# Optimization experiments

Measured on AMD Instinct MI355X. Metric: run time of the kernel, lower is better.

The kernel has to match this reference:

```python
import jax, jax.numpy as jnp
import numpy as np

B, S, D, H, E, K = 4, 1024, 1024, 4096, 8, 2


def setup_inputs() -> dict:
    key = jax.random.key(0)
    ks = jax.random.split(key, 10)
    s = 0.02
    return {
        "x": jax.random.normal(ks[0], (B, S, D), jnp.float32),
        "noise": jax.random.normal(ks[1], (B, S, E), jnp.float32),
        "Wg": jax.random.normal(ks[2], (D, E), jnp.float32) * s,
        "bg": jnp.zeros((E,), jnp.float32),
        "Wn": jax.random.normal(ks[3], (D, E), jnp.float32) * s,
        "bn": jnp.zeros((E,), jnp.float32),
        "W1": jax.random.normal(ks[4], (E, D, H), jnp.float32) * s,
        "b1": jnp.zeros((E, H), jnp.float32),
        "W2": jax.random.normal(ks[5], (E, H, D), jnp.float32) * s,
        "b2": jnp.zeros((E, D), jnp.float32),
    }


def reference(x, noise, Wg, bg, Wn, bn, W1, b1, W2, b2):
    # --- noisy top-k gating ---
    logits = x @ Wg + bg                                   # [B,S,E]
    noisy = logits + noise * jax.nn.softplus(x @ Wn + bn)  # [B,S,E]
    topk_vals, topk_idx = jax.lax.top_k(noisy, K)          # [B,S,K]
    weights = jax.nn.softmax(topk_vals, axis=-1)           # [B,S,K]
    oh = jax.nn.one_hot(topk_idx, E, dtype=x.dtype)        # [B,S,K,E]
    mask = oh.sum(axis=-2)                                 # [B,S,E] 0/1 (topk idx distinct)
    w_full = (weights[..., None] * oh).sum(axis=-2)        # [B,S,E] combine weights

    # --- per-expert FFN (dense over experts, selected via w_full) ---
    h = jax.nn.gelu(jnp.einsum('bsd,edh->bseh', x, W1) + b1, approximate=False)
    eout = jnp.einsum('bseh,ehd->bsed', h, W2) + b2        # [B,S,E,D]
    combined = jnp.einsum('bse,bsed->bsd', w_full, eout)   # [B,S,D]

    # --- load balancing loss on clean gate probs ---
    gate_probs = jax.nn.softmax(logits, axis=-1)           # [B,S,E]
    expert_count = mask.sum(axis=(0, 1))                   # [E]
    total_tokens = mask.sum()
    expert_util = expert_count / total_tokens
    load_loss = jnp.sum(expert_util * gate_probs.mean(axis=(0, 1))) * E
    return combined, load_loss
```

## Files before the change

kernel.cpp:

```cpp
#include <hip/hip_runtime.h>
#include <hip/hip_bf16.h>

#define T_TOK 4096
#define D_DIM 1024
#define H_DIM 4096
#define E_EXP 8
#define K_TOP 2
#define TP (T_TOK * K_TOP)
#define BM 128
#define BN 128
#define BKS 32
#define MAX_TILES 72

typedef __attribute__((ext_vector_type(8))) short bf16x8;
typedef __attribute__((ext_vector_type(4))) float f32x4;
typedef __attribute__((ext_vector_type(8))) unsigned short u16x8;
typedef __attribute__((ext_vector_type(4))) unsigned short u16x4;

#define SWZ(row, chunk) ((chunk) ^ (((row) >> 1) & 3))

static __device__ __forceinline__ void gload16(const unsigned short* g, unsigned short* l) {
  __builtin_amdgcn_global_load_lds((const __attribute__((address_space(1))) void*)g,
                                   (__attribute__((address_space(3))) void*)l, 16, 0, 0);
}

static __device__ __forceinline__ unsigned short f2bf(float f) {
  unsigned int bits = __float_as_uint(f);
  unsigned int lsb = (bits >> 16) & 1u;
  bits += 0x7fffu + lsb;
  return (unsigned short)(bits >> 16);
}

static __device__ __forceinline__ float gelu_fast(float u) {
  float z = u * (0.79788456080286536f + 0.0356774081f * u * u);
  float t = __expf(-2.f * z);
  return u / (1.f + t);
}

__global__ __launch_bounds__(256) void convert_x_kernel(
    const float* __restrict__ x, unsigned short* __restrict__ xb) {
  int idx = blockIdx.x * 256 + threadIdx.x;
  float4 v = ((const float4*)x)[idx];
  u16x4 o;
  o[0] = f2bf(v.x); o[1] = f2bf(v.y); o[2] = f2bf(v.z); o[3] = f2bf(v.w);
  *(u16x4*)(xb + (size_t)idx * 4) = o;
}

__global__ __launch_bounds__(256) void transpose_bf16_kernel(
    const float* __restrict__ src, unsigned short* __restrict__ dst, int R, int C) {
  __shared__ float tile[32][33];
  const int e = blockIdx.z;
  const int c0 = blockIdx.x * 32, r0 = blockIdx.y * 32;
  const int tx = threadIdx.x, ty = threadIdx.y;
  const float* s = src + (size_t)e * R * C;
  unsigned short* d = dst + (size_t)e * R * C;
#pragma unroll
  for (int j = 0; j < 4; ++j)
    tile[ty + 8 * j][tx] = s[(size_t)(r0 + ty + 8 * j) * C + c0 + tx];
  __syncthreads();
#pragma unroll
  for (int j = 0; j < 4; ++j)
    d[(size_t)(c0 + ty + 8 * j) * R + r0 + tx] = f2bf(tile[tx][ty + 8 * j]);
}

__global__ __launch_bounds__(256) void gating_kernel(
    const float* __restrict__ x, const float* __restrict__ noise,
    const float* __restrict__ Wg, const float* __restrict__ bg,
    const float* __restrict__ Wn, const float* __restrict__ bn,
    int* __restrict__ tok_e, float* __restrict__ tok_w,
    float* __restrict__ gp_tok, int* __restrict__ counts) {
  const int tid = threadIdx.x, lane = tid & 63, wid = tid >> 6;
  const int t = blockIdx.x * 4 + wid;
  const float* xrow = x + (size_t)t * D_DIM;
  float ag[8] = {0, 0, 0, 0, 0, 0, 0, 0};
  float an[8] = {0, 0, 0, 0, 0, 0, 0, 0};
#pragma unroll 4
  for (int i = 0; i < 16; ++i) {
    int dd = i * 64 + lane;
    float xv = xrow[dd];
    const float4* g4 = (const float4*)(Wg + (size_t)dd * 8);
    const float4* n4 = (const float4*)(Wn + (size_t)dd * 8);
    float4 ga = g4[0], gb = g4[1], na = n4[0], nb = n4[1];
    ag[0] += xv * ga.x; ag[1] += xv * ga.y; ag[2] += xv * ga.z; ag[3] += xv * ga.w;
    ag[4] += xv * gb.x; ag[5] += xv * gb.y; ag[6] += xv * gb.z; ag[7] += xv * gb.w;
    an[0] += xv * na.x; an[1] += xv * na.y; an[2] += xv * na.z; an[3] += xv * na.w;
    an[4] += xv * nb.x; an[5] += xv * nb.y; an[6] += xv * nb.z; an[7] += xv * nb.w;
  }
#pragma unroll
  for (int e = 0; e < 8; ++e) {
    for (int off = 32; off > 0; off >>= 1) {
      ag[e] += __shfl_down(ag[e], off);
      an[e] += __shfl_down(an[e], off);
    }
  }
  if (lane == 0) {
    float logit[8], noisy[8];
#pragma unroll
    for (int e = 0; e < 8; ++e) {
      logit[e] = ag[e] + bg[e];
      float pre = an[e] + bn[e];
      float sp = fmaxf(pre, 0.f) + log1pf(expf(-fabsf(pre)));
      noisy[e] = logit[e] + noise[(size_t)t * 8 + e] * sp;
    }
    float mx = logit[0];
#pragma unroll
    for (int e = 1; e < 8; ++e) mx = fmaxf(mx, logit[e]);
    float s = 0.f, p[8];
#pragma unroll
    for (int e = 0; e < 8; ++e) { p[e] = expf(logit[e] - mx); s += p[e]; }
    float inv = 1.f / s;
#pragma unroll
    for (int e = 0; e < 8; ++e) gp_tok[(size_t)t * 8 + e] = p[e] * inv;
    int i0 = 0; float v0 = noisy[0];
#pragma unroll
    for (int e = 1; e < 8; ++e) if (noisy[e] > v0) { v0 = noisy[e]; i0 = e; }
    int i1 = -1; float v1 = 0.f;
#pragma unroll
    for (int e = 0; e < 8; ++e) {
      if (e == i0) continue;
      if (i1 < 0 || noisy[e] > v1) { v1 = noisy[e]; i1 = e; }
    }
    float e1 = expf(v1 - v0);
    float w0 = 1.f / (1.f + e1);
    float w1 = e1 * w0;
    tok_e[t * 2 + 0] = i0; tok_e[t * 2 + 1] = i1;
    tok_w[t * 2 + 0] = w0; tok_w[t * 2 + 1] = w1;
    atomicAdd(&counts[i0], 1);
    atomicAdd(&counts[i1], 1);
  }
}

__global__ void scan_kernel(const int* __restrict__ counts, int* __restrict__ offsets,
                            int* __restrict__ cursor, int4* __restrict__ tiles,
                            int* __restrict__ ntiles) {
  if (threadIdx.x == 0 && blockIdx.x == 0) {
    int off = 0, nt = 0;
    for (int e = 0; e < E_EXP; ++e) {
      offsets[e] = off;
      int c = counts[e];
      for (int r = 0; r < c; r += BM) {
        tiles[nt] = make_int4(e, off + r, min(BM, c - r), 0);
        ++nt;
      }
      off += c;
      cursor[e] = 0;
    }
    offsets[E_EXP] = off;
    *ntiles = nt;
  }
}

__global__ __launch_bounds__(256) void scatter_kernel(
    const int* __restrict__ tok_e, const float* __restrict__ tok_w,
    const int* __restrict__ offsets, int* __restrict__ cursor,
    int* __restrict__ pair_token, float* __restrict__ pair_w) {
  int t = blockIdx.x * 256 + threadIdx.x;
  if (t >= T_TOK) return;
#pragma unroll
  for (int k = 0; k < 2; ++k) {
    int e = tok_e[t * 2 + k];
    int pos = atomicAdd(&cursor[e], 1);
    int p = offsets[e] + pos;
    pair_token[p] = t;
    pair_w[p] = tok_w[t * 2 + k];
  }
}

__global__ __launch_bounds__(256) void ffn1_kernel(
    const unsigned short* __restrict__ xb,
    const unsigned short* __restrict__ w1t,
    const float* __restrict__ b1,
    const int* __restrict__ pair_token,
    const int4* __restrict__ tiles, const int* __restrict__ ntiles,
    unsigned short* __restrict__ hbuf) {
  const int NB = H_DIM / BN;
  const int nwg = MAX_TILES * NB;
  int bid = blockIdx.x;
  int wg = (bid & 7) * (nwg >> 3) + (bid >> 3);
  int tileId = wg / NB, nb = wg - tileId * NB;
  if (tileId >= *ntiles) return;
  int4 tl = tiles[tileId];
  const int e = tl.x, row0 = tl.y, rows = tl.z;
  const int n0 = nb * BN;

  __shared__ unsigned short As[BM * BKS];
  __shared__ unsigned short Bs[BN * BKS];

  const int tid = threadIdx.x;
  const int wid = tid >> 6, lane = tid & 63;
  const int sr = tid >> 2;
  const int sc = tid & 3;
  const int scz = SWZ(sr, sc) * 8;

  int r0a = row0 + sr;       if (r0a > TP - 1) r0a = TP - 1;
  int r1a = row0 + sr + 64;  if (r1a > TP - 1) r1a = TP - 1;
  const unsigned short* a0 = xb + (size_t)pair_token[r0a] * D_DIM + scz;
  const unsigned short* a1 = xb + (size_t)pair_token[r1a] * D_DIM + scz;
  const unsigned short* bp0 = w1t + ((size_t)e * H_DIM + (n0 + sr)) * D_DIM + scz;
  const unsigned short* bp1 = w1t + ((size_t)e * H_DIM + (n0 + sr + 64)) * D_DIM + scz;

  unsigned short* AsW = As + wid * 512;
  unsigned short* BsW = Bs + wid * 512;

  const int wr = wid >> 1, wc = wid & 1;
  const int lrow = lane & 15, lkc = lane >> 4;

  f32x4 acc[4][4] = {};

  for (int k0 = 0; k0 < D_DIM; k0 += BKS) {
    gload16(a0 + k0, AsW);
    gload16(a1 + k0, AsW + 2048);
    gload16(bp0 + k0, BsW);
    gload16(bp1 + k0, BsW + 2048);
    __syncthreads();
    bf16x8 af[4], bfr[4];
#pragma unroll
    for (int m = 0; m < 4; ++m) {
      int r = wr * 64 + m * 16 + lrow;
      af[m] = *(const bf16x8*)(&As[r * BKS + SWZ(r, lkc) * 8]);
    }
#pragma unroll
    for (int n = 0; n < 4; ++n) {
      int r = wc * 64 + n * 16 + lrow;
      bfr[n] = *(const bf16x8*)(&Bs[r * BKS + SWZ(r, lkc) * 8]);
    }
#pragma unroll
    for (int m = 0; m < 4; ++m)
#pragma unroll
      for (int n = 0; n < 4; ++n)
        acc[m][n] = __builtin_amdgcn_mfma_f32_16x16x32_bf16(af[m], bfr[n], acc[m][n], 0, 0, 0);
    __syncthreads();
  }

  const int colbase = n0 + wc * 64;
#pragma unroll
  for (int n = 0; n < 4; ++n) {
    int colg = colbase + n * 16 + lrow;
    float bias = b1[(size_t)e * H_DIM + colg];
#pragma unroll
    for (int m = 0; m < 4; ++m) {
      int rbase = wr * 64 + m * 16 + (lane >> 4) * 4;
#pragma unroll
      for (int j = 0; j < 4; ++j) {
        int rloc = rbase + j;
        if (rloc < rows) {
          float v = acc[m][n][j] + bias;
          hbuf[(size_t)(row0 + rloc) * H_DIM + colg] = f2bf(gelu_fast(v));
        }
      }
    }
  }
}

__global__ __launch_bounds__(256) void ffn2_kernel(
    const unsigned short* __restrict__ hbuf,
    const unsigned short* __restrict__ w2t,
    const float* __restrict__ b2,
    const int* __restrict__ pair_token, const float* __restrict__ pair_w,
    const int4* __restrict__ tiles, const int* __restrict__ ntiles,
    float* __restrict__ out) {
  const int NB = D_DIM / BN;
  const int nwg = MAX_TILES * NB;
  int bid = blockIdx.x;
  int wg = (bid & 7) * (nwg >> 3) + (bid >> 3);
  int tileId = wg / NB, nb = wg - tileId * NB;
  if (tileId >= *ntiles) return;
  int4 tl = tiles[tileId];
  const int e = tl.x, row0 = tl.y, rows = tl.z;
  const int n0 = nb * BN;

  __shared__ unsigned short As[BM * BKS];
  __shared__ unsigned short Bs[BN * BKS];
  __shared__ int stok[BM];
  __shared__ float spw[BM];

  const int tid = threadIdx.x;
  if (tid < BM) {
    int rr = row0 + tid; if (rr > TP - 1) rr = TP - 1;
    stok[tid] = pair_token[rr];
    spw[tid] = pair_w[rr];
  }

  const int wid = tid >> 6, lane = tid & 63;
  const int sr = tid >> 2;
  const int sc = tid & 3;
  const int scz = SWZ(sr, sc) * 8;

  int r0a = row0 + sr;       if (r0a > TP - 1) r0a = TP - 1;
  int r1a = row0 + sr + 64;  if (r1a > TP - 1) r1a = TP - 1;
  const unsigned short* a0 = hbuf + (size_t)r0a * H_DIM + scz;
  const unsigned short* a1 = hbuf + (size_t)r1a * H_DIM + scz;
  const unsigned short* bp0 = w2t + ((size_t)e * D_DIM + (n0 + sr)) * H_DIM + scz;
  const unsigned short* bp1 = w2t + ((size_t)e * D_DIM + (n0 + sr + 64)) * H_DIM + scz;

  unsigned short* AsW = As + wid * 512;
  unsigned short* BsW = Bs + wid * 512;

  const int wr = wid >> 1, wc = wid & 1;
  const int lrow = lane & 15, lkc = lane >> 4;

  f32x4 acc[4][4] = {};

  for (int k0 = 0; k0 < H_DIM; k0 += BKS) {
    gload16(a0 + k0, AsW);
    gload16(a1 + k0, AsW + 2048);
    gload16(bp0 + k0, BsW);
    gload16(bp1 + k0, BsW + 2048);
    __syncthreads();
    bf16x8 af[4], bfr[4];
#pragma unroll
    for (int m = 0; m < 4; ++m) {
      int r = wr * 64 + m * 16 + lrow;
      af[m] = *(const bf16x8*)(&As[r * BKS + SWZ(r, lkc) * 8]);
    }
#pragma unroll
    for (int n = 0; n < 4; ++n) {
      int r = wc * 64 + n * 16 + lrow;
      bfr[n] = *(const bf16x8*)(&Bs[r * BKS + SWZ(r, lkc) * 8]);
    }
#pragma unroll
    for (int m = 0; m < 4; ++m)
#pragma unroll
      for (int n = 0; n < 4; ++n)
        acc[m][n] = __builtin_amdgcn_mfma_f32_16x16x32_bf16(af[m], bfr[n], acc[m][n], 0, 0, 0);
    __syncthreads();
  }

  const int colbase = n0 + wc * 64;
#pragma unroll
  for (int n = 0; n < 4; ++n) {
    int colg = colbase + n * 16 + lrow;
    float bias = b2[(size_t)e * D_DIM + colg];
#pragma unroll
    for (int m = 0; m < 4; ++m) {
      int rbase = wr * 64 + m * 16 + (lane >> 4) * 4;
#pragma unroll
      for (int j = 0; j < 4; ++j) {
        int rloc = rbase + j;
        if (rloc < rows) {
          float v = acc[m][n][j] + bias;
          unsafeAtomicAdd(&out[(size_t)stok[rloc] * D_DIM + colg], spw[rloc] * v);
        }
      }
    }
  }
}

__global__ __launch_bounds__(256) void loss_kernel(
    const float* __restrict__ gp_tok, const int* __restrict__ counts,
    float* __restrict__ out) {
  __shared__ float red[256];
  const int tid = threadIdx.x;
  float part[8] = {0, 0, 0, 0, 0, 0, 0, 0};
  for (int r = tid; r < T_TOK; r += 256) {
    const float* g = gp_tok + (size_t)r * 8;
#pragma unroll
    for (int e = 0; e < 8; ++e) part[e] += g[e];
  }
  float total[8];
#pragma unroll
  for (int e = 0; e < 8; ++e) {
    red[tid] = part[e];
    __syncthreads();
    for (int s = 128; s > 0; s >>= 1) {
      if (tid < s) red[tid] += red[tid + s];
      __syncthreads();
    }
    if (tid == 0) total[e] = red[0];
    __syncthreads();
  }
  if (tid == 0) {
    float ll = 0.f;
#pragma unroll
    for (int e = 0; e < 8; ++e)
      ll += ((float)counts[e] / (float)TP) * (total[e] / (float)T_TOK);
    out[(size_t)T_TOK * D_DIM] = ll * (float)E_EXP;
  }
}

extern "C" void kernel_launch(void* const* d_in, const int* in_sizes, int n_in,
                              void* d_out, int out_size, void* d_ws, size_t ws_size,
                              hipStream_t stream) {
  (void)in_sizes; (void)n_in; (void)ws_size;
  const float* x     = (const float*)d_in[0];
  const float* noise = (const float*)d_in[1];
  const float* Wg    = (const float*)d_in[2];
  const float* bg    = (const float*)d_in[3];
  const float* Wn    = (const float*)d_in[4];
  const float* bn    = (const float*)d_in[5];
  const float* W1    = (const float*)d_in[6];
  const float* b1    = (const float*)d_in[7];
  const float* W2    = (const float*)d_in[8];
  const float* b2    = (const float*)d_in[9];
  float* out = (float*)d_out;

  char* ws = (char*)d_ws;
  size_t o = 0;
  auto take = [&](size_t b) { size_t r = o; o += (b + 255) & ~(size_t)255; return r; };
  int*   counts     = (int*)(ws + take(16 * 4));
  int*   cursor     = counts + 8;
  int*   offsets    = (int*)(ws + take(9 * 4));
  int*   ntiles     = (int*)(ws + take(4));
  int4*  tiles      = (int4*)(ws + take(MAX_TILES * 16));
  int*   tok_e      = (int*)(ws + take((size_t)TP * 4));
  float* tok_w      = (float*)(ws + take((size_t)TP * 4));
  float* gp_tok     = (float*)(ws + take((size_t)T_TOK * 8 * 4));
  int*   pair_token = (int*)(ws + take((size_t)TP * 4));
  float* pair_w     = (float*)(ws + take((size_t)TP * 4));
  unsigned short* xb  = (unsigned short*)(ws + take((size_t)T_TOK * D_DIM * 2));
  unsigned short* w1t = (unsigned short*)(ws + take((size_t)E_EXP * H_DIM * D_DIM * 2));
  unsigned short* w2t = (unsigned short*)(ws + take((size_t)E_EXP * H_DIM * D_DIM * 2));
  unsigned short* hbuf = (unsigned short*)(ws + take((size_t)TP * H_DIM * 2));

  hipMemsetAsync(d_out, 0, (size_t)out_size * sizeof(float), stream);
  hipMemsetAsync(counts, 0, 16 * 4, stream);

  convert_x_kernel<<<(T_TOK * D_DIM) / (256 * 4), 256, 0, stream>>>(x, xb);
  transpose_bf16_kernel<<<dim3(H_DIM / 32, D_DIM / 32, E_EXP), dim3(32, 8), 0, stream>>>(
      W1, w1t, D_DIM, H_DIM);
  transpose_bf16_kernel<<<dim3(D_DIM / 32, H_DIM / 32, E_EXP), dim3(32, 8), 0, stream>>>(
      W2, w2t, H_DIM, D_DIM);
  gating_kernel<<<T_TOK / 4, 256, 0, stream>>>(x, noise, Wg, bg, Wn, bn,
                                               tok_e, tok_w, gp_tok, counts);
  scan_kernel<<<1, 64, 0, stream>>>(counts, offsets, cursor, tiles, ntiles);
  scatter_kernel<<<T_TOK / 256, 256, 0, stream>>>(tok_e, tok_w, offsets, cursor,
                                                  pair_token, pair_w);
  ffn1_kernel<<<dim3(MAX_TILES * (H_DIM / BN)), 256, 0, stream>>>(
      xb, w1t, b1, pair_token, tiles, ntiles, hbuf);
  ffn2_kernel<<<dim3(MAX_TILES * (D_DIM / BN)), 256, 0, stream>>>(
      hbuf, w2t, b2, pair_token, pair_w, tiles, ntiles, out);
  loss_kernel<<<1, 256, 0, stream>>>(gp_tok, counts, out);
}
```

Measured before the change: 523.3 us.

## Double-buffer LDS tiles in expert GEMMs and vectorize weight transpose stores

The FFN1 and FFN2 grouped GEMM kernels now use two LDS buffers and issue the async global-to-LDS loads for the next K-slice before computing on the current one. This removes one barrier per iteration and lets memory latency overlap with MFMA work. The weight transpose kernel now handles 128x32 tiles and writes eight bf16 values per 16-byte store, which cuts store transactions. The cost is twice the LDS per GEMM block, which may lower occupancy.

New measurement: 555.8 us. +6.2%, slower.

```diff
diff --git a/kernel.cpp b/kernel.cpp
--- a/kernel.cpp
+++ b/kernel.cpp
@@ -48,19 +48,27 @@
 
 __global__ __launch_bounds__(256) void transpose_bf16_kernel(
     const float* __restrict__ src, unsigned short* __restrict__ dst, int R, int C) {
-  __shared__ float tile[32][33];
+  __shared__ float tile[32][129];
   const int e = blockIdx.z;
-  const int c0 = blockIdx.x * 32, r0 = blockIdx.y * 32;
-  const int tx = threadIdx.x, ty = threadIdx.y;
+  const int c0 = blockIdx.x * 32, r0 = blockIdx.y * 128;
+  const int tx = threadIdx.x & 31, ty = threadIdx.x >> 5;
   const float* s = src + (size_t)e * R * C;
   unsigned short* d = dst + (size_t)e * R * C;
 #pragma unroll
-  for (int j = 0; j < 4; ++j)
-    tile[ty + 8 * j][tx] = s[(size_t)(r0 + ty + 8 * j) * C + c0 + tx];
+  for (int j = 0; j < 16; ++j) {
+    int r = ty + 8 * j;
+    tile[tx][r] = s[(size_t)(r0 + r) * C + c0 + tx];
+  }
   __syncthreads();
-#pragma unroll
-  for (int j = 0; j < 4; ++j)
-    d[(size_t)(c0 + ty + 8 * j) * R + r0 + tx] = f2bf(tile[tx][ty + 8 * j]);
+  const int wc = threadIdx.x & 15, cc = threadIdx.x >> 4;
+#pragma unroll
+  for (int half = 0; half < 2; ++half) {
+    int col = cc + 16 * half;
+    u16x8 o;
+#pragma unroll
+    for (int q = 0; q < 8; ++q) o[q] = f2bf(tile[col][wc * 8 + q]);
+    *(u16x8*)(&d[(size_t)(c0 + col) * R + r0 + wc * 8]) = o;
+  }
 }
 
 __global__ __launch_bounds__(256) void gating_kernel(
@@ -183,8 +191,8 @@
   const int e = tl.x, row0 = tl.y, rows = tl.z;
   const int n0 = nb * BN;
 
-  __shared__ unsigned short As[BM * BKS];
-  __shared__ unsigned short Bs[BN * BKS];
+  __shared__ unsigned short As[2][BM * BKS];
+  __shared__ unsigned short Bs[2][BN * BKS];
 
   const int tid = threadIdx.x;
   const int wid = tid >> 6, lane = tid & 63;
@@ -199,30 +207,37 @@
   const unsigned short* bp0 = w1t + ((size_t)e * H_DIM + (n0 + sr)) * D_DIM + scz;
   const unsigned short* bp1 = w1t + ((size_t)e * H_DIM + (n0 + sr + 64)) * D_DIM + scz;
 
-  unsigned short* AsW = As + wid * 512;
-  unsigned short* BsW = Bs + wid * 512;
-
+  const int wbase = wid * 512;
   const int wr = wid >> 1, wc = wid & 1;
   const int lrow = lane & 15, lkc = lane >> 4;
 
   f32x4 acc[4][4] = {};
 
+  gload16(a0, &As[0][wbase]);
+  gload16(a1, &As[0][wbase + 2048]);
+  gload16(bp0, &Bs[0][wbase]);
+  gload16(bp1, &Bs[0][wbase + 2048]);
+  __syncthreads();
+
+  int cur = 0;
   for (int k0 = 0; k0 < D_DIM; k0 += BKS) {
-    gload16(a0 + k0, AsW);
-    gload16(a1 + k0, AsW + 2048);
-    gload16(bp0 + k0, BsW);
-    gload16(bp1 + k0, BsW + 2048);
-    __syncthreads();
+    int nxt = cur ^ 1;
+    if (k0 + BKS < D_DIM) {
+      gload16(a0 + k0 + BKS, &As[nxt][wbase]);
+      gload16(a1 + k0 + BKS, &As[nxt][wbase + 2048]);
+      gload16(bp0 + k0 + BKS, &Bs[nxt][wbase]);
+      gload16(bp1 + k0 + BKS, &Bs[nxt][wbase + 2048]);
+    }
     bf16x8 af[4], bfr[4];
 #pragma unroll
     for (int m = 0; m < 4; ++m) {
       int r = wr * 64 + m * 16 + lrow;
-      af[m] = *(const bf16x8*)(&As[r * BKS + SWZ(r, lkc) * 8]);
+      af[m] = *(const bf16x8*)(&As[cur][r * BKS + SWZ(r, lkc) * 8]);
     }
 #pragma unroll
     for (int n = 0; n < 4; ++n) {
       int r = wc * 64 + n * 16 + lrow;
-      bfr[n] = *(const bf16x8*)(&Bs[r * BKS + SWZ(r, lkc) * 8]);
+      bfr[n] = *(const bf16x8*)(&Bs[cur][r * BKS + SWZ(r, lkc) * 8]);
     }
 #pragma unroll
     for (int m = 0; m < 4; ++m)
@@ -230,6 +245,7 @@
       for (int n = 0; n < 4; ++n)
         acc[m][n] = __builtin_amdgcn_mfma_f32_16x16x32_bf16(af[m], bfr[n], acc[m][n], 0, 0, 0);
     __syncthreads();
+    cur = nxt;
   }
 
   const int colbase = n0 + wc * 64;
@@ -269,8 +285,8 @@
   const int e = tl.x, row0 = tl.y, rows = tl.z;
   const int n0 = nb * BN;
 
-  __shared__ unsigned short As[BM * BKS];
-  __shared__ unsigned short Bs[BN * BKS];
+  __shared__ unsigned short As[2][BM * BKS];
+  __shared__ unsigned short Bs[2][BN * BKS];
   __shared__ int stok[BM];
   __shared__ float spw[BM];
 
@@ -293,30 +309,37 @@
   const unsigned short* bp0 = w2t + ((size_t)e * D_DIM + (n0 + sr)) * H_DIM + scz;
   const unsigned short* bp1 = w2t + ((size_t)e * D_DIM + (n0 + sr + 64)) * H_DIM + scz;
 
-  unsigned short* AsW = As + wid * 512;
-  unsigned short* BsW = Bs + wid * 512;
-
+  const int wbase = wid * 512;
   const int wr = wid >> 1, wc = wid & 1;
   const int lrow = lane & 15, lkc = lane >> 4;
 
   f32x4 acc[4][4] = {};
 
+  gload16(a0, &As[0][wbase]);
+  gload16(a1, &As[0][wbase + 2048]);
+  gload16(bp0, &Bs[0][wbase]);
+  gload16(bp1, &Bs[0][wbase + 2048]);
+  __syncthreads();
+
+  int cur = 0;
   for (int k0 = 0; k0 < H_DIM; k0 += BKS) {
-    gload16(a0 + k0, AsW);
-    gload16(a1 + k0, AsW + 2048);
-    gload16(bp0 + k0, BsW);
-    gload16(bp1 + k0, BsW + 2048);
-    __syncthreads();
+    int nxt = cur ^ 1;
+    if (k0 + BKS < H_DIM) {
+      gload16(a0 + k0 + BKS, &As[nxt][wbase]);
+      gload16(a1 + k0 + BKS, &As[nxt][wbase + 2048]);
+      gload16(bp0 + k0 + BKS, &Bs[nxt][wbase]);
+      gload16(bp1 + k0 + BKS, &Bs[nxt][wbase + 2048]);
+    }
     bf16x8 af[4], bfr[4];
 #pragma unroll
     for (int m = 0; m < 4; ++m) {
       int r = wr * 64 + m * 16 + lrow;
-      af[m] = *(const bf16x8*)(&As[r * BKS + SWZ(r, lkc) * 8]);
+      af[m] = *(const bf16x8*)(&As[cur][r * BKS + SWZ(r, lkc) * 8]);
     }
 #pragma unroll
     for (int n = 0; n < 4; ++n) {
       int r = wc * 64 + n * 16 + lrow;
-      bfr[n] = *(const bf16x8*)(&Bs[r * BKS + SWZ(r, lkc) * 8]);
+      bfr[n] = *(const bf16x8*)(&Bs[cur][r * BKS + SWZ(r, lkc) * 8]);
     }
 #pragma unroll
     for (int m = 0; m < 4; ++m)
@@ -324,6 +347,7 @@
       for (int n = 0; n < 4; ++n)
         acc[m][n] = __builtin_amdgcn_mfma_f32_16x16x32_bf16(af[m], bfr[n], acc[m][n], 0, 0, 0);
     __syncthreads();
+    cur = nxt;
   }
 
   const int colbase = n0 + wc * 64;
@@ -416,9 +440,9 @@
   hipMemsetAsync(counts, 0, 16 * 4, stream);
 
   convert_x_kernel<<<(T_TOK * D_DIM) / (256 * 4), 256, 0, stream>>>(x, xb);
-  transpose_bf16_kernel<<<dim3(H_DIM / 32, D_DIM / 32, E_EXP), dim3(32, 8), 0, stream>>>(
+  transpose_bf16_kernel<<<dim3(H_DIM / 32, D_DIM / 128, E_EXP), 256, 0, stream>>>(
       W1, w1t, D_DIM, H_DIM);
-  transpose_bf16_kernel<<<dim3(D_DIM / 32, H_DIM / 32, E_EXP), dim3(32, 8), 0, stream>>>(
+  transpose_bf16_kernel<<<dim3(D_DIM / 32, H_DIM / 128, E_EXP), 256, 0, stream>>>(
       W2, w2t, H_DIM, D_DIM);
   gating_kernel<<<T_TOK / 4, 256, 0, stream>>>(x, noise, Wg, bg, Wn, bn,
                                                tok_e, tok_w, gp_tok, counts);
```
